# Kernel tuning notes

Measured on AMD Instinct MI355X. Metric: run time of the kernel, lower is better.

## Reference

```python
import jax, jax.numpy as jnp
import numpy as np
import math

B, S, D, H = 2, 2048, 1024, 16
DK = D // H


def setup_inputs() -> dict:
    key = jax.random.key(0)
    ks = jax.random.split(key, 12)
    std = 1.0 / math.sqrt(D)
    inp = {
        "q": jax.random.normal(ks[0], (B, S, D), jnp.float32),
        "k": jax.random.normal(ks[1], (B, S, D), jnp.float32),
        "v": jax.random.normal(ks[2], (B, S, D), jnp.float32),
        # causal mask, broadcast over batch and heads
        "mask": jnp.tril(jnp.ones((S, S), jnp.int32))[None, None, :, :],
        "wq": jax.random.normal(ks[3], (D, D), jnp.float32) * std,
        "bq": jax.random.normal(ks[4], (D,), jnp.float32) * std,
        "wk": jax.random.normal(ks[5], (D, D), jnp.float32) * std,
        "bk": jax.random.normal(ks[6], (D,), jnp.float32) * std,
        "wv": jax.random.normal(ks[7], (D, D), jnp.float32) * std,
        "bv": jax.random.normal(ks[8], (D,), jnp.float32) * std,
        "wo": jax.random.normal(ks[9], (D, D), jnp.float32) * std,
        "bo": jax.random.normal(ks[10], (D,), jnp.float32) * std,
    }
    return inp


def _split_heads(x):
    # [B,S,D] -> [B,H,S,DK]
    b, s, _ = x.shape
    return x.reshape(b, s, H, DK).transpose(0, 2, 1, 3)


def reference(q, k, v, mask, wq, bq, wk, bk, wv, bv, wo, bo):
    # nn.Linear: y = x @ W^T + b
    query = _split_heads(q @ wq.T + bq)
    key_h = _split_heads(k @ wk.T + bk)
    value = _split_heads(v @ wv.T + bv)

    scale = 1.0 / math.sqrt(DK)
    scores = jnp.einsum("bhqd,bhkd->bhqk", query, key_h) * scale  # [B,H,S,S]
    scores = jnp.where(mask == 0, jnp.float32(-1e9), scores)
    attn = jax.nn.softmax(scores, axis=-1)  # dropout p=0.0 -> identity

    x = jnp.einsum("bhqk,bhkd->bhqd", attn, value)  # [B,H,S,DK]
    x = x.transpose(0, 2, 1, 3).reshape(q.shape[0], -1, H * DK)  # [B,S,D]
    return x @ wo.T + bo
```

## Files before the change

### kernel.cpp

```cpp
#include <hip/hip_runtime.h>

#define B_SZ    2
#define S_LEN   2048
#define D_MODEL 1024
#define H_NUM   16
#define DK_H    64
#define M_ROWS  (B_SZ * S_LEN)

typedef __attribute__((ext_vector_type(8))) short  short8;
typedef __attribute__((ext_vector_type(4))) short  short4v;
typedef __attribute__((ext_vector_type(4))) float  floatx4;

__device__ __forceinline__ short f2b(float f) {
    union { float f; unsigned u; } x; x.f = f;
    unsigned u = x.u + 0x7fffu + ((x.u >> 16) & 1u);
    return (short)(u >> 16);
}
__device__ __forceinline__ short f2b_t(float f) {
    union { float f; unsigned u; } x; x.f = f;
    return (short)(x.u >> 16);
}

typedef __attribute__((address_space(1))) const unsigned int gu32;
typedef __attribute__((address_space(3))) unsigned int       lu32;
__device__ __forceinline__ void gload_lds16(const short* g, short* l) {
    __builtin_amdgcn_global_load_lds((gu32*)g, (lu32*)l, 16, 0, 0);
}

#define QSCALE 0.18033688011112042f
#define SM_SHIFT 12.0f

__global__ void cvt3_kernel(const float* __restrict__ i0, const float* __restrict__ i1,
                            const float* __restrict__ i2,
                            short* __restrict__ o0, short* __restrict__ o1, short* __restrict__ o2) {
    const float* in  = (blockIdx.y == 0) ? i0 : (blockIdx.y == 1) ? i1 : i2;
    short*       out = (blockIdx.y == 0) ? o0 : (blockIdx.y == 1) ? o1 : o2;
    int i = (blockIdx.x * 256 + threadIdx.x) * 4;
    float4 v = *(const float4*)(in + i);
    short4v r;
    r[0] = f2b(v.x); r[1] = f2b(v.y); r[2] = f2b(v.z); r[3] = f2b(v.w);
    *(short4v*)(out + i) = r;
}

__global__ void cvt4_kernel(const float* __restrict__ i0, const float* __restrict__ i1,
                            const float* __restrict__ i2, const float* __restrict__ i3,
                            short* __restrict__ o0, short* __restrict__ o1,
                            short* __restrict__ o2, short* __restrict__ o3) {
    const float* in  = (blockIdx.y == 0) ? i0 : (blockIdx.y == 1) ? i1 : (blockIdx.y == 2) ? i2 : i3;
    short*       out = (blockIdx.y == 0) ? o0 : (blockIdx.y == 1) ? o1 : (blockIdx.y == 2) ? o2 : o3;
    int i = (blockIdx.x * 256 + threadIdx.x) * 4;
    float4 v = *(const float4*)(in + i);
    short4v r;
    r[0] = f2b(v.x); r[1] = f2b(v.y); r[2] = f2b(v.z); r[3] = f2b(v.w);
    *(short4v*)(out + i) = r;
}

__global__ __launch_bounds__(256)
void gemm_qkv_kernel(const short* __restrict__ xq, const short* __restrict__ xk,
                     const short* __restrict__ xv,
                     const short* __restrict__ wq, const short* __restrict__ wk,
                     const short* __restrict__ wv,
                     const float* __restrict__ bq, const float* __restrict__ bk,
                     const float* __restrict__ bv,
                     short* __restrict__ Qp, short* __restrict__ Kp, short* __restrict__ Vt)
{
    __shared__ short sa[128 * 32];
    __shared__ short sb[128 * 32];

    const int which = blockIdx.y >> 3;
    const short* A    = (which == 0) ? xq : (which == 1) ? xk : xv;
    const short* W    = (which == 0) ? wq : (which == 1) ? wk : wv;
    const float* bias = (which == 0) ? bq : (which == 1) ? bk : bv;
    const float scale = (which == 0) ? QSCALE : 1.0f;

    const int nb = (blockIdx.y & 7) * 128;
    const int m0 = blockIdx.x * 128;
    const int t = threadIdx.x, wave = t >> 6, lane = t & 63;
    const int quad = lane >> 4, l16 = lane & 15;
    const int wm = (wave & 1) * 64, wn = (wave >> 1) * 64;

    const int r0 = t >> 2, cs = t & 3;
    const int c0 = cs ^ ((r0 >> 1) & 3);
    const short* Ab0 = A + (size_t)(m0 + r0) * D_MODEL + c0 * 8;
    const short* Ab1 = Ab0 + (size_t)64 * D_MODEL;
    const short* Bb0 = W + (size_t)(nb + r0) * D_MODEL + c0 * 8;
    const short* Bb1 = Bb0 + (size_t)64 * D_MODEL;
    short* sa0 = sa + t * 8;  short* sa1 = sa + 2048 + t * 8;
    short* sb0 = sb + t * 8;  short* sb1 = sb + 2048 + t * 8;

    int a_off[4], b_off[4];
#pragma unroll
    for (int i = 0; i < 4; ++i) {
        int ar = wm + i * 16 + l16;
        a_off[i] = ar * 32 + ((quad ^ ((ar >> 1) & 3)) * 8);
        int br = wn + i * 16 + l16;
        b_off[i] = br * 32 + ((quad ^ ((br >> 1) & 3)) * 8);
    }

    floatx4 acc[4][4] = {};
    for (int k0 = 0; k0 < D_MODEL; k0 += 32) {
        __syncthreads();
        gload_lds16(Ab0 + k0, sa0);
        gload_lds16(Ab1 + k0, sa1);
        gload_lds16(Bb0 + k0, sb0);
        gload_lds16(Bb1 + k0, sb1);
        __syncthreads();
        short8 af[4], bf[4];
#pragma unroll
        for (int i = 0; i < 4; ++i) af[i] = *(const short8*)(sa + a_off[i]);
#pragma unroll
        for (int i = 0; i < 4; ++i) bf[i] = *(const short8*)(sb + b_off[i]);
#pragma unroll
        for (int mt = 0; mt < 4; ++mt)
#pragma unroll
            for (int nt = 0; nt < 4; ++nt)
                acc[mt][nt] = __builtin_amdgcn_mfma_f32_16x16x32_bf16(af[mt], bf[nt], acc[mt][nt], 0, 0, 0);
    }

#pragma unroll
    for (int nt = 0; nt < 4; ++nt) {
        int ncol = nb + wn + nt * 16 + l16;
        int h = ncol >> 6, dk = ncol & 63;
        float bv_ = bias[ncol];
#pragma unroll
        for (int mt = 0; mt < 4; ++mt) {
            int mrow0 = m0 + wm + mt * 16 + quad * 4;
            int bb = mrow0 >> 11, s0 = mrow0 & (S_LEN - 1);
            if (which < 2) {
                short* Out = (which == 0) ? Qp : Kp;
#pragma unroll
                for (int r = 0; r < 4; ++r) {
                    float v = (acc[mt][nt][r] + bv_) * scale;
                    Out[(((size_t)bb * H_NUM + h) * S_LEN + (s0 + r)) * DK_H + dk] = f2b(v);
                }
            } else {
                short4v pk;
#pragma unroll
                for (int r = 0; r < 4; ++r) pk[r] = f2b(acc[mt][nt][r] + bv_);
                *(short4v*)(&Vt[(((size_t)bb * H_NUM + h) * DK_H + dk) * S_LEN + s0]) = pk;
            }
        }
    }
}

__global__ __launch_bounds__(512, 2)
void attn_kernel(const short* __restrict__ Qp, const short* __restrict__ Kp,
                 const short* __restrict__ Vt, short* __restrict__ Xa)
{
    __shared__ short pl[8][16 * 72];

    const int bh = blockIdx.y;
    const int t = threadIdx.x, wave = t >> 6, lane = t & 63;
    const int quad = lane >> 4, l16 = lane & 15;
    const int tile = (wave < 4) ? (int)blockIdx.x : (15 - (int)blockIdx.x);
    const int wv = wave & 3;

    const short* Qb  = Qp + (size_t)bh * S_LEN * DK_H;
    const short* Kb  = Kp + (size_t)bh * S_LEN * DK_H;
    const short* Vtb = Vt + (size_t)bh * DK_H * S_LEN;

    const int q0 = tile * 128 + wv * 32;
    const int ktimax = (q0 + 31) >> 6;

    short8 qf[2][2];
#pragma unroll
    for (int g = 0; g < 2; ++g)
#pragma unroll
        for (int ks = 0; ks < 2; ++ks)
            qf[g][ks] = *(const short8*)(Qb + (size_t)(q0 + g * 16 + l16) * DK_H + ks * 32 + quad * 8);

    short8 bl = {};
    if (l16 == 0) {
#pragma unroll
        for (int j = 0; j < 8; ++j) bl[j] = (short)0x3F80;
    }

    floatx4 o[2][4] = {};
    floatx4 ol[2] = {};
    short* plw = &pl[wave][0];

    short8 bk0[4][2], bk1[4][2];
#pragma unroll
    for (int nt = 0; nt < 4; ++nt)
#pragma unroll
        for (int ks = 0; ks < 2; ++ks)
            bk0[nt][ks] = *(const short8*)(Kb + (size_t)(nt * 16 + l16) * DK_H + ks * 32 + quad * 8);

    auto step = [&](int kti, short8 (&bkc)[4][2], short8 (&bkn)[4][2]) {
        const int kbase = kti * 64;

        floatx4 sc[2][4] = {};
#pragma unroll
        for (int g = 0; g < 2; ++g)
#pragma unroll
            for (int nt = 0; nt < 4; ++nt)
#pragma unroll
                for (int ks = 0; ks < 2; ++ks)
                    sc[g][nt] = __builtin_amdgcn_mfma_f32_16x16x32_bf16(qf[g][ks], bkc[nt][ks], sc[g][nt], 0, 0, 0);

        if (kti < ktimax) {
#pragma unroll
            for (int nt = 0; nt < 4; ++nt)
#pragma unroll
                for (int ks = 0; ks < 2; ++ks)
                    bkn[nt][ks] = *(const short8*)(Kb + (size_t)(kbase + 64 + nt * 16 + l16) * DK_H + ks * 32 + quad * 8);
        }

        short8 bv[4][2];
#pragma unroll
        for (int nt = 0; nt < 4; ++nt)
#pragma unroll
            for (int ks = 0; ks < 2; ++ks)
                bv[nt][ks] = *(const short8*)(Vtb + (size_t)(nt * 16 + l16) * S_LEN + kbase + ks * 32 + quad * 8);

        const bool diag = (kti == ktimax);

#pragma unroll
        for (int g = 0; g < 2; ++g) {
            const int qg = q0 + g * 16 + quad * 4;
            if (diag) {
#pragma unroll
                for (int nt = 0; nt < 4; ++nt) {
                    int key = kbase + nt * 16 + l16;
#pragma unroll
                    for (int r = 0; r < 4; ++r)
                        if (key > qg + r) sc[g][nt][r] = -1e30f;
                }
            }

#pragma unroll
            for (int nt = 0; nt < 4; ++nt)
#pragma unroll
                for (int r = 0; r < 4; ++r)
                    plw[(quad * 4 + r) * 72 + nt * 16 + l16] = f2b_t(exp2f(sc[g][nt][r] - SM_SHIFT));

            short8 ap0 = *(const short8*)(plw + l16 * 72 + quad * 8);
            short8 ap1 = *(const short8*)(plw + l16 * 72 + 32 + quad * 8);

#pragma unroll
            for (int nt = 0; nt < 4; ++nt) {
                o[g][nt] = __builtin_amdgcn_mfma_f32_16x16x32_bf16(ap0, bv[nt][0], o[g][nt], 0, 0, 0);
                o[g][nt] = __builtin_amdgcn_mfma_f32_16x16x32_bf16(ap1, bv[nt][1], o[g][nt], 0, 0, 0);
            }
            ol[g] = __builtin_amdgcn_mfma_f32_16x16x32_bf16(ap0, bl, ol[g], 0, 0, 0);
            ol[g] = __builtin_amdgcn_mfma_f32_16x16x32_bf16(ap1, bl, ol[g], 0, 0, 0);
        }
    };

    for (int kti = 0; kti <= ktimax; ) {
        step(kti, bk0, bk1);
        ++kti;
        if (kti <= ktimax) {
            step(kti, bk1, bk0);
            ++kti;
        }
    }

    const int b_ = bh >> 4, h = bh & 15;
#pragma unroll
    for (int g = 0; g < 2; ++g) {
#pragma unroll
        for (int r = 0; r < 4; ++r) {
            float lsum = __shfl(ol[g][r], (lane & 48));
            float rinv = 1.0f / lsum;
            int srow = q0 + g * 16 + quad * 4 + r;
#pragma unroll
            for (int nt = 0; nt < 4; ++nt) {
                int col = h * 64 + nt * 16 + l16;
                Xa[((size_t)b_ * S_LEN + srow) * D_MODEL + col] = f2b(o[g][nt][r] * rinv);
            }
        }
    }
}

__global__ __launch_bounds__(256)
void gemm_out_kernel(const short* __restrict__ A, const short* __restrict__ W,
                     const float* __restrict__ bias, float* __restrict__ out)
{
    __shared__ short sa[128 * 32];
    __shared__ short sb[128 * 32];

    const int nb = blockIdx.y * 128;
    const int m0 = blockIdx.x * 128;
    const int t = threadIdx.x, wave = t >> 6, lane = t & 63;
    const int quad = lane >> 4, l16 = lane & 15;
    const int wm = (wave & 1) * 64, wn = (wave >> 1) * 64;

    const int r0 = t >> 2, cs = t & 3;
    const int c0 = cs ^ ((r0 >> 1) & 3);
    const short* Ab0 = A + (size_t)(m0 + r0) * D_MODEL + c0 * 8;
    const short* Ab1 = Ab0 + (size_t)64 * D_MODEL;
    const short* Bb0 = W + (size_t)(nb + r0) * D_MODEL + c0 * 8;
    const short* Bb1 = Bb0 + (size_t)64 * D_MODEL;
    short* sa0 = sa + t * 8;  short* sa1 = sa + 2048 + t * 8;
    short* sb0 = sb + t * 8;  short* sb1 = sb + 2048 + t * 8;

    int a_off[4], b_off[4];
#pragma unroll
    for (int i = 0; i < 4; ++i) {
        int ar = wm + i * 16 + l16;
        a_off[i] = ar * 32 + ((quad ^ ((ar >> 1) & 3)) * 8);
        int br = wn + i * 16 + l16;
        b_off[i] = br * 32 + ((quad ^ ((br >> 1) & 3)) * 8);
    }

    floatx4 acc[4][4] = {};
    for (int k0 = 0; k0 < D_MODEL; k0 += 32) {
        __syncthreads();
        gload_lds16(Ab0 + k0, sa0);
        gload_lds16(Ab1 + k0, sa1);
        gload_lds16(Bb0 + k0, sb0);
        gload_lds16(Bb1 + k0, sb1);
        __syncthreads();
        short8 af[4], bf[4];
#pragma unroll
        for (int i = 0; i < 4; ++i) af[i] = *(const short8*)(sa + a_off[i]);
#pragma unroll
        for (int i = 0; i < 4; ++i) bf[i] = *(const short8*)(sb + b_off[i]);
#pragma unroll
        for (int mt = 0; mt < 4; ++mt)
#pragma unroll
            for (int nt = 0; nt < 4; ++nt)
                acc[mt][nt] = __builtin_amdgcn_mfma_f32_16x16x32_bf16(af[mt], bf[nt], acc[mt][nt], 0, 0, 0);
    }

#pragma unroll
    for (int nt = 0; nt < 4; ++nt) {
        int ncol = nb + wn + nt * 16 + l16;
        float bv_ = bias[ncol];
#pragma unroll
        for (int mt = 0; mt < 4; ++mt) {
            int mrow0 = m0 + wm + mt * 16 + quad * 4;
#pragma unroll
            for (int r = 0; r < 4; ++r)
                out[(size_t)(mrow0 + r) * D_MODEL + ncol] = acc[mt][nt][r] + bv_;
        }
    }
}

extern "C" void kernel_launch(void* const* d_in, const int* in_sizes, int n_in,
                              void* d_out, int out_size, void* d_ws, size_t ws_size,
                              hipStream_t stream)
{
    (void)in_sizes; (void)n_in; (void)out_size; (void)ws_size;
    const float* q  = (const float*)d_in[0];
    const float* k  = (const float*)d_in[1];
    const float* v  = (const float*)d_in[2];
    const float* wq = (const float*)d_in[4];
    const float* bq = (const float*)d_in[5];
    const float* wk = (const float*)d_in[6];
    const float* bk = (const float*)d_in[7];
    const float* wv = (const float*)d_in[8];
    const float* bv = (const float*)d_in[9];
    const float* wo = (const float*)d_in[10];
    const float* bo = (const float*)d_in[11];
    float* out = (float*)d_out;

    const size_t XE = (size_t)M_ROWS * D_MODEL;
    const size_t WE = (size_t)D_MODEL * D_MODEL;
    short* ws_  = (short*)d_ws;
    short* xq_b = ws_;
    short* xk_b = xq_b + XE;
    short* xv_b = xk_b + XE;
    short* wq_b = xv_b + XE;
    short* wk_b = wq_b + WE;
    short* wv_b = wk_b + WE;
    short* wo_b = wv_b + WE;
    short* Qp   = wo_b + WE;
    short* Kp   = Qp + XE;
    short* Vt   = Kp + XE;
    short* Xa   = xq_b;

    dim3 blk(256);
    cvt3_kernel<<<dim3((unsigned)(XE / 1024), 3), blk, 0, stream>>>(q, k, v, xq_b, xk_b, xv_b);
    cvt4_kernel<<<dim3((unsigned)(WE / 1024), 4), blk, 0, stream>>>(wq, wk, wv, wo, wq_b, wk_b, wv_b, wo_b);

    gemm_qkv_kernel<<<dim3(M_ROWS / 128, 24), blk, 0, stream>>>(
        xq_b, xk_b, xv_b, wq_b, wk_b, wv_b, bq, bk, bv, Qp, Kp, Vt);

    attn_kernel<<<dim3(8, B_SZ * H_NUM), dim3(512), 0, stream>>>(Qp, Kp, Vt, Xa);

    gemm_out_kernel<<<dim3(M_ROWS / 128, D_MODEL / 128), blk, 0, stream>>>(Xa, wo_b, bo, out);
}
```

Baseline: 261.9 us.

## Merge conversion kernels, prefetch V tiles, and remap attention block order

Combines the two fp32-to-bf16 conversion launches into one kernel in which activation blocks loop over four strided chunks, removing a launch. In the attention kernel, V fragments are now double-buffered and prefetched one key tile ahead, alongside K, to hide global load latency, at the cost of more registers under the 512-thread, 2-block launch bound. The attention block index is also linearized so that consecutive blocks cover different heads instead of tiles of the same head, which changes scheduling and cache locality.

```diff
diff --git a/kernel.cpp b/kernel.cpp
--- a/kernel.cpp
+++ b/kernel.cpp
@@ -30,29 +30,36 @@
 #define QSCALE 0.18033688011112042f
 #define SM_SHIFT 12.0f
 
-__global__ void cvt3_kernel(const float* __restrict__ i0, const float* __restrict__ i1,
-                            const float* __restrict__ i2,
-                            short* __restrict__ o0, short* __restrict__ o1, short* __restrict__ o2) {
-    const float* in  = (blockIdx.y == 0) ? i0 : (blockIdx.y == 1) ? i1 : i2;
-    short*       out = (blockIdx.y == 0) ? o0 : (blockIdx.y == 1) ? o1 : o2;
-    int i = (blockIdx.x * 256 + threadIdx.x) * 4;
-    float4 v = *(const float4*)(in + i);
-    short4v r;
-    r[0] = f2b(v.x); r[1] = f2b(v.y); r[2] = f2b(v.z); r[3] = f2b(v.w);
-    *(short4v*)(out + i) = r;
-}
-
-__global__ void cvt4_kernel(const float* __restrict__ i0, const float* __restrict__ i1,
-                            const float* __restrict__ i2, const float* __restrict__ i3,
-                            short* __restrict__ o0, short* __restrict__ o1,
-                            short* __restrict__ o2, short* __restrict__ o3) {
-    const float* in  = (blockIdx.y == 0) ? i0 : (blockIdx.y == 1) ? i1 : (blockIdx.y == 2) ? i2 : i3;
-    short*       out = (blockIdx.y == 0) ? o0 : (blockIdx.y == 1) ? o1 : (blockIdx.y == 2) ? o2 : o3;
-    int i = (blockIdx.x * 256 + threadIdx.x) * 4;
-    float4 v = *(const float4*)(in + i);
-    short4v r;
-    r[0] = f2b(v.x); r[1] = f2b(v.y); r[2] = f2b(v.z); r[3] = f2b(v.w);
-    *(short4v*)(out + i) = r;
+__global__ void cvt_all_kernel(const float* __restrict__ xq, const float* __restrict__ xk,
+                               const float* __restrict__ xv, const float* __restrict__ wq,
+                               const float* __restrict__ wk, const float* __restrict__ wv,
+                               const float* __restrict__ wo,
+                               short* __restrict__ oxq, short* __restrict__ oxk,
+                               short* __restrict__ oxv, short* __restrict__ owq,
+                               short* __restrict__ owk, short* __restrict__ owv,
+                               short* __restrict__ owo)
+{
+    const int y = blockIdx.y;
+    const float* in;
+    short* out;
+    switch (y) {
+        case 0: in = xq; out = oxq; break;
+        case 1: in = xk; out = oxk; break;
+        case 2: in = xv; out = oxv; break;
+        case 3: in = wq; out = owq; break;
+        case 4: in = wk; out = owk; break;
+        case 5: in = wv; out = owv; break;
+        default: in = (y == 6) ? wo : wv; out = (y == 6) ? owo : owv; break;
+    }
+    const int npass = (y < 3) ? 4 : 1;
+    int base = blockIdx.x * 1024 + threadIdx.x * 4;
+    for (int p = 0; p < npass; ++p) {
+        int i = base + p * 1048576;
+        float4 v = *(const float4*)(in + i);
+        short4v r;
+        r[0] = f2b(v.x); r[1] = f2b(v.y); r[2] = f2b(v.z); r[3] = f2b(v.w);
+        *(short4v*)(out + i) = r;
+    }
 }
 
 __global__ __launch_bounds__(256)
@@ -149,10 +156,12 @@
 {
     __shared__ short pl[8][16 * 72];
 
-    const int bh = blockIdx.y;
+    const int c = (int)(blockIdx.x + 8 * blockIdx.y);
+    const int bh = c & 31;
+    const int pairtile = c >> 5;
     const int t = threadIdx.x, wave = t >> 6, lane = t & 63;
     const int quad = lane >> 4, l16 = lane & 15;
-    const int tile = (wave < 4) ? (int)blockIdx.x : (15 - (int)blockIdx.x);
+    const int tile = (wave < 4) ? pairtile : (15 - pairtile);
     const int wv = wave & 3;
 
     const short* Qb  = Qp + (size_t)bh * S_LEN * DK_H;
@@ -179,14 +188,17 @@
     floatx4 ol[2] = {};
     short* plw = &pl[wave][0];
 
-    short8 bk0[4][2], bk1[4][2];
+    short8 bk0[4][2], bk1[4][2], bv0[4][2], bv1[4][2];
 #pragma unroll
     for (int nt = 0; nt < 4; ++nt)
 #pragma unroll
-        for (int ks = 0; ks < 2; ++ks)
+        for (int ks = 0; ks < 2; ++ks) {
             bk0[nt][ks] = *(const short8*)(Kb + (size_t)(nt * 16 + l16) * DK_H + ks * 32 + quad * 8);
-
-    auto step = [&](int kti, short8 (&bkc)[4][2], short8 (&bkn)[4][2]) {
+            bv0[nt][ks] = *(const short8*)(Vtb + (size_t)(nt * 16 + l16) * S_LEN + ks * 32 + quad * 8);
+        }
+
+    auto step = [&](int kti, short8 (&bkc)[4][2], short8 (&bkn)[4][2],
+                    short8 (&bvc)[4][2], short8 (&bvn)[4][2]) {
         const int kbase = kti * 64;
 
         floatx4 sc[2][4] = {};
@@ -202,16 +214,11 @@
 #pragma unroll
             for (int nt = 0; nt < 4; ++nt)
 #pragma unroll
-                for (int ks = 0; ks < 2; ++ks)
+                for (int ks = 0; ks < 2; ++ks) {
                     bkn[nt][ks] = *(const short8*)(Kb + (size_t)(kbase + 64 + nt * 16 + l16) * DK_H + ks * 32 + quad * 8);
-        }
-
-        short8 bv[4][2];
-#pragma unroll
-        for (int nt = 0; nt < 4; ++nt)
-#pragma unroll
-            for (int ks = 0; ks < 2; ++ks)
-                bv[nt][ks] = *(const short8*)(Vtb + (size_t)(nt * 16 + l16) * S_LEN + kbase + ks * 32 + quad * 8);
+                    bvn[nt][ks] = *(const short8*)(Vtb + (size_t)(nt * 16 + l16) * S_LEN + kbase + 64 + ks * 32 + quad * 8);
+                }
+        }
 
         const bool diag = (kti == ktimax);
 
@@ -239,8 +246,8 @@
 
 #pragma unroll
             for (int nt = 0; nt < 4; ++nt) {
-                o[g][nt] = __builtin_amdgcn_mfma_f32_16x16x32_bf16(ap0, bv[nt][0], o[g][nt], 0, 0, 0);
-                o[g][nt] = __builtin_amdgcn_mfma_f32_16x16x32_bf16(ap1, bv[nt][1], o[g][nt], 0, 0, 0);
+                o[g][nt] = __builtin_amdgcn_mfma_f32_16x16x32_bf16(ap0, bvc[nt][0], o[g][nt], 0, 0, 0);
+                o[g][nt] = __builtin_amdgcn_mfma_f32_16x16x32_bf16(ap1, bvc[nt][1], o[g][nt], 0, 0, 0);
             }
             ol[g] = __builtin_amdgcn_mfma_f32_16x16x32_bf16(ap0, bl, ol[g], 0, 0, 0);
             ol[g] = __builtin_amdgcn_mfma_f32_16x16x32_bf16(ap1, bl, ol[g], 0, 0, 0);
@@ -248,10 +255,10 @@
     };
 
     for (int kti = 0; kti <= ktimax; ) {
-        step(kti, bk0, bk1);
+        step(kti, bk0, bk1, bv0, bv1);
         ++kti;
         if (kti <= ktimax) {
-            step(kti, bk1, bk0);
+            step(kti, bk1, bk0, bv1, bv0);
             ++kti;
         }
     }
@@ -372,8 +379,8 @@
     short* Xa   = xq_b;
 
     dim3 blk(256);
-    cvt3_kernel<<<dim3((unsigned)(XE / 1024), 3), blk, 0, stream>>>(q, k, v, xq_b, xk_b, xv_b);
-    cvt4_kernel<<<dim3((unsigned)(WE / 1024), 4), blk, 0, stream>>>(wq, wk, wv, wo, wq_b, wk_b, wv_b, wo_b);
+    cvt_all_kernel<<<dim3(1024, 7), blk, 0, stream>>>(
+        q, k, v, wq, wk, wv, wo, xq_b, xk_b, xv_b, wq_b, wk_b, wv_b, wo_b);
 
     gemm_qkv_kernel<<<dim3(M_ROWS / 128, 24), blk, 0, stream>>>(
         xq_b, xk_b, xv_b, wq_b, wk_b, wv_b, bq, bk, bv, Qp, Kp, Vt);
```

Result: slower. 272.5 us (+4.0%).
